# Performance work log

Hardware: AMD Instinct MI355X
Metric: run time of the kernel (lower is better)

Reference implementation:

```python
import jax, jax.numpy as jnp
import numpy as np

B, N, NC, T, C, H = 8, 16, 16, 64, 512, 8


def setup_inputs() -> dict:
    key = jax.random.key(0)
    ks = jax.random.split(key, 7)
    s = 1.0 / np.sqrt(C)  # ~kaiming-uniform scale for Linear weights
    x = jax.random.normal(ks[0], (B, N, T, C), dtype=jnp.float32)
    c = jax.random.normal(ks[1], (B, NC, T, C), dtype=jnp.float32)
    mask = jax.random.randint(ks[2], (B, N * T, (N + NC) * T), 0, 2).astype(bool)
    Wq = jax.random.normal(ks[3], (C, C), dtype=jnp.float32) * s  # [out, in], torch Linear layout
    Wk = jax.random.normal(ks[4], (C, C), dtype=jnp.float32) * s
    Wv = jax.random.normal(ks[5], (C, C), dtype=jnp.float32) * s
    Wp = jax.random.normal(ks[6], (C, C), dtype=jnp.float32) * s
    return {"x": x, "c": c, "mask": mask, "Wq": Wq, "Wk": Wk, "Wv": Wv, "Wp": Wp}


def reference(x, c, mask, Wq, Wk, Wv, Wp):
    Bx, Nx, Tx, Cx = x.shape
    Dh = Cx // H
    kv_in = jnp.concatenate([x, c], axis=1)           # hybrid: [B, N+NC, T, C]
    Nk = kv_in.shape[1]
    # torch Linear: y = x @ W.T  -> einsum '...c,dc->...d'
    q = jnp.einsum('bntc,dc->bntd', x, Wq).reshape(Bx, Nx * Tx, H, Dh).transpose(0, 2, 1, 3)
    k = jnp.einsum('bntc,dc->bntd', kv_in, Wk).reshape(Bx, Nk * Tx, H, Dh).transpose(0, 2, 1, 3)
    v = jnp.einsum('bntc,dc->bntd', kv_in, Wv).reshape(Bx, Nk * Tx, H, Dh).transpose(0, 2, 1, 3)
    att = jnp.einsum('bhqd,bhkd->bhqk', q, k) * (1.0 / np.sqrt(Dh))  # [B,H,NT,NkT]
    att = jnp.where(mask[:, None, :, :], -jnp.inf, att)
    att = jax.nn.softmax(att, axis=-1)
    y = jnp.einsum('bhqk,bhkd->bhqd', att, v)          # [B,H,NT,Dh]
    y = y.transpose(0, 2, 1, 3).reshape(Bx, Nx * Tx, Cx)
    y = jnp.einsum('btc,dc->btd', y, Wp)
    return y.reshape(Bx, Nx, Tx, Cx)
```

## Files before the change

### kernel.cpp

```cpp
#include <hip/hip_runtime.h>
#include <hip/hip_bf16.h>
#include <stdint.h>

typedef __bf16 v8bf __attribute__((ext_vector_type(8)));
typedef float f32x4 __attribute__((ext_vector_type(4)));

__device__ __forceinline__ void gload_lds16(const void* g, void* l) {
    __builtin_amdgcn_global_load_lds(
        (const __attribute__((address_space(1))) void*)g,
        (__attribute__((address_space(3))) void*)l, 16, 0, 0);
}

__device__ __forceinline__ unsigned short f2bf(float f) {
    __hip_bfloat16 h = __float2bfloat16(f);
    return __builtin_bit_cast(unsigned short, h);
}

__global__ __launch_bounds__(256) void cvt_xcw(const float* __restrict__ x,
                                               const float* __restrict__ c,
                                               const float* __restrict__ wq,
                                               const float* __restrict__ wk,
                                               const float* __restrict__ wv,
                                               const float* __restrict__ wp,
                                               __hip_bfloat16* __restrict__ xc,
                                               __hip_bfloat16* __restrict__ wout) {
    int bid = blockIdx.x;
    if (bid < 8192) {
        int i = bid * 256 + threadIdx.x;
        long e = (long)i * 4;
        int b = (int)(e >> 20);
        int rem = (int)(e & ((1 << 20) - 1));
        int r = rem >> 9;
        int col = rem & 511;
        const float* src = (r < 1024) ? (x + ((long)b << 19) + (long)r * 512 + col)
                                      : (c + ((long)b << 19) + (long)(r - 1024) * 512 + col);
        float4 v = *(const float4*)src;
        ushort4 o;
        o.x = f2bf(v.x); o.y = f2bf(v.y); o.z = f2bf(v.z); o.w = f2bf(v.w);
        ((ushort4*)xc)[i] = o;
    } else {
        int i = (bid - 8192) * 256 + threadIdx.x;
        int e = i * 4;
        int w = e >> 18;
        int off = e & ((1 << 18) - 1);
        const float* src = (w == 0 ? wq : w == 1 ? wk : w == 2 ? wv : wp) + off;
        float4 val = *(const float4*)src;
        ushort4 o;
        o.x = f2bf(val.x); o.y = f2bf(val.y); o.z = f2bf(val.z); o.w = f2bf(val.w);
        ((ushort4*)wout)[i] = o;
    }
}

__global__ __launch_bounds__(256) void cvt_mask(const int* __restrict__ mask,
                                                unsigned long long* __restrict__ mb) {
    int t = threadIdx.x;
    long base = (long)blockIdx.x * 1024;
#pragma unroll
    for (int j = 0; j < 4; j++) {
        long i = base + j * 256 + t;
        int v = mask[i] != 0;
        unsigned long long bits = __ballot(v);
        if ((t & 63) == 0) mb[i >> 6] = bits;
    }
}

__global__ __launch_bounds__(256) void gemm_qkv(const __hip_bfloat16* __restrict__ A,
                                                const __hip_bfloat16* __restrict__ Bw,
                                                __hip_bfloat16* __restrict__ Qw,
                                                __hip_bfloat16* __restrict__ Kw,
                                                __hip_bfloat16* __restrict__ Vtw) {
    __shared__ union {
        struct { __hip_bfloat16 As[128 * 32]; __hip_bfloat16 Bs[128 * 32]; } s;
        __hip_bfloat16 T[128 * 136];
    } u;
    const int tid = threadIdx.x;
    const int wave = tid >> 6, lane = tid & 63;
    const int m0 = blockIdx.x * 128, n0 = blockIdx.y * 128;

    const int la = lane >> 2;
    const int kc = (lane & 3) * 8;
    const long ga0 = (long)(m0 + wave * 16 + la) * 512 + kc;
    const long ga1 = (long)(m0 + (wave + 4) * 16 + la) * 512 + kc;
    const long gb0 = (long)(n0 + wave * 16 + la) * 512 + kc;
    const long gb1 = (long)(n0 + (wave + 4) * 16 + la) * 512 + kc;

    f32x4 acc[4][4] = {};
    const int mw = (wave & 1) * 64, nw = (wave >> 1) * 64;
    const int lrow = lane & 15, lk = (lane >> 4) * 8;

    for (int k0 = 0; k0 < 512; k0 += 32) {
        gload_lds16(A + ga0 + k0, &u.s.As[wave * 512]);
        gload_lds16(A + ga1 + k0, &u.s.As[(wave + 4) * 512]);
        gload_lds16(Bw + gb0 + k0, &u.s.Bs[wave * 512]);
        gload_lds16(Bw + gb1 + k0, &u.s.Bs[(wave + 4) * 512]);
        __syncthreads();
        v8bf a[4], b[4];
#pragma unroll
        for (int i = 0; i < 4; i++) {
            a[i] = *(const v8bf*)&u.s.As[(mw + i * 16 + lrow) * 32 + lk];
            b[i] = *(const v8bf*)&u.s.Bs[(nw + i * 16 + lrow) * 32 + lk];
        }
#pragma unroll
        for (int mi = 0; mi < 4; mi++)
#pragma unroll
            for (int ni = 0; ni < 4; ni++)
                acc[mi][ni] = __builtin_amdgcn_mfma_f32_16x16x32_bf16(a[mi], b[ni], acc[mi][ni], 0, 0, 0);
        __syncthreads();
    }

    const int lq = lane >> 4;
    if (blockIdx.y < 8) {
#pragma unroll
        for (int mi = 0; mi < 4; mi++)
#pragma unroll
            for (int ni = 0; ni < 4; ni++)
#pragma unroll
                for (int r = 0; r < 4; r++) {
                    int grow = m0 + mw + mi * 16 + lq * 4 + r;
                    int gcol = n0 + nw + ni * 16 + lrow;
                    int w = gcol >> 9, g9 = gcol & 511;
                    int h = g9 >> 6, dh = g9 & 63;
                    int b_ = grow >> 11, rr = grow & 2047;
                    __hip_bfloat16 bv = __float2bfloat16(acc[mi][ni][r]);
                    if (w == 0) {
                        if (rr < 1024)
                            Qw[((long)(b_ * 8 + h) * 1024 + rr) * 64 + dh] = bv;
                    } else {
                        Kw[((long)(b_ * 8 + h) * 2048 + rr) * 64 + dh] = bv;
                    }
                }
    } else {
#pragma unroll
        for (int mi = 0; mi < 4; mi++)
#pragma unroll
            for (int ni = 0; ni < 4; ni++) {
                int n_l = nw + ni * 16 + lrow;
                int m_l = mw + mi * 16 + lq * 4;
                ushort4 pk;
                pk.x = f2bf(acc[mi][ni][0]); pk.y = f2bf(acc[mi][ni][1]);
                pk.z = f2bf(acc[mi][ni][2]); pk.w = f2bf(acc[mi][ni][3]);
                *(ushort4*)&u.T[n_l * 136 + m_l] = pk;
            }
        __syncthreads();
        const int no = (blockIdx.y - 8) * 128;
        const int b_ = m0 >> 11, rrb = m0 & 2047;
#pragma unroll
        for (int i = 0; i < 8; i++) {
            int s = tid + i * 256;
            int n_l = s >> 4, ch = s & 15;
            int ng = no + n_l;
            int h = ng >> 6, dh = ng & 63;
            uint4 v = *(const uint4*)&u.T[n_l * 136 + ch * 8];
            *(uint4*)&Vtw[((long)(b_ * 8 + h) * 64 + dh) * 2048 + rrb + ch * 8] = v;
        }
    }
}

__global__ __launch_bounds__(256) void gemm_out(const __hip_bfloat16* __restrict__ A,
                                                const __hip_bfloat16* __restrict__ Bw,
                                                float* __restrict__ outp) {
    __shared__ __hip_bfloat16 As[128 * 32];
    __shared__ __hip_bfloat16 Bs[128 * 32];
    const int tid = threadIdx.x;
    const int wave = tid >> 6, lane = tid & 63;
    const int m0 = blockIdx.x * 128, n0 = blockIdx.y * 128;

    const int la = lane >> 2;
    const int kc = (lane & 3) * 8;
    const long ga0 = (long)(m0 + wave * 16 + la) * 512 + kc;
    const long ga1 = (long)(m0 + (wave + 4) * 16 + la) * 512 + kc;
    const long gb0 = (long)(n0 + wave * 16 + la) * 512 + kc;
    const long gb1 = (long)(n0 + (wave + 4) * 16 + la) * 512 + kc;

    f32x4 acc[4][4] = {};
    const int mw = (wave & 1) * 64, nw = (wave >> 1) * 64;
    const int lrow = lane & 15, lk = (lane >> 4) * 8;

    for (int k0 = 0; k0 < 512; k0 += 32) {
        gload_lds16(A + ga0 + k0, &As[wave * 512]);
        gload_lds16(A + ga1 + k0, &As[(wave + 4) * 512]);
        gload_lds16(Bw + gb0 + k0, &Bs[wave * 512]);
        gload_lds16(Bw + gb1 + k0, &Bs[(wave + 4) * 512]);
        __syncthreads();
        v8bf a[4], b[4];
#pragma unroll
        for (int i = 0; i < 4; i++) {
            a[i] = *(const v8bf*)&As[(mw + i * 16 + lrow) * 32 + lk];
            b[i] = *(const v8bf*)&Bs[(nw + i * 16 + lrow) * 32 + lk];
        }
#pragma unroll
        for (int mi = 0; mi < 4; mi++)
#pragma unroll
            for (int ni = 0; ni < 4; ni++)
                acc[mi][ni] = __builtin_amdgcn_mfma_f32_16x16x32_bf16(a[mi], b[ni], acc[mi][ni], 0, 0, 0);
        __syncthreads();
    }

    const int lq = lane >> 4;
#pragma unroll
    for (int mi = 0; mi < 4; mi++)
#pragma unroll
        for (int ni = 0; ni < 4; ni++)
#pragma unroll
            for (int r = 0; r < 4; r++) {
                int grow = m0 + mw + mi * 16 + lq * 4 + r;
                int gcol = n0 + nw + ni * 16 + lrow;
                outp[(long)grow * 512 + gcol] = acc[mi][ni][r];
            }
}

__global__ __launch_bounds__(256) void flash(const __hip_bfloat16* __restrict__ Q,
                                             const __hip_bfloat16* __restrict__ K,
                                             const __hip_bfloat16* __restrict__ Vt,
                                             const unsigned long long* __restrict__ Mb,
                                             __hip_bfloat16* __restrict__ Y) {
    __shared__ __hip_bfloat16 Ps[4][64 * 32];
    __shared__ float Ls[4][64];

    const int L = blockIdx.x;
    const int b = L & 7, h = L >> 7, qt = (L >> 3) & 15;
    const int bh = b * 8 + h;
    const int tid = threadIdx.x, w = tid >> 6, lane = tid & 63;
    const int lcol = lane & 15, lq = lane >> 4;

    const __hip_bfloat16* Qp = Q + ((long)bh * 1024 + qt * 64) * 64;
    const __hip_bfloat16* Kp = K + ((long)bh * 2048 + w * 16 + lcol) * 64;
    const __hip_bfloat16* Vp = Vt + (long)bh * 64 * 2048;
    const unsigned long long* Mp = Mb + ((long)b * 1024 + qt * 64) * 32;

    v8bf bq[4][2];
#pragma unroll
    for (int mi = 0; mi < 4; mi++)
#pragma unroll
        for (int ks = 0; ks < 2; ks++)
            bq[mi][ks] = *(const v8bf*)(Qp + (mi * 16 + lcol) * 64 + ks * 32 + lq * 8);

    f32x4 Oacc[4][4] = {};
    float lsum[4] = {0.f, 0.f, 0.f, 0.f};
    const int vkey = (lq >> 1) * 64 + w * 16 + (lq & 1) * 8;
    const int mshift = w * 16 + lq * 4;

    for (int kt = 0; kt < 16; kt++) {
        unsigned long long mb_[4][2];
#pragma unroll
        for (int mi = 0; mi < 4; mi++)
#pragma unroll
            for (int kt2 = 0; kt2 < 2; kt2++)
                mb_[mi][kt2] = Mp[(mi * 16 + lcol) * 32 + kt * 2 + kt2] >> mshift;

        v8bf ak[2][2];
#pragma unroll
        for (int kt2 = 0; kt2 < 2; kt2++)
#pragma unroll
            for (int ks = 0; ks < 2; ks++)
                ak[kt2][ks] = *(const v8bf*)(Kp + (long)(kt * 128 + kt2 * 64) * 64 + ks * 32 + lq * 8);

        v8bf bv[4];
#pragma unroll
        for (int nd = 0; nd < 4; nd++)
            bv[nd] = *(const v8bf*)(Vp + (long)(nd * 16 + lcol) * 2048 + kt * 128 + vkey);

#pragma unroll
        for (int kt2 = 0; kt2 < 2; kt2++)
#pragma unroll
            for (int mi = 0; mi < 4; mi++) {
                f32x4 st = {};
                st = __builtin_amdgcn_mfma_f32_16x16x32_bf16(ak[kt2][0], bq[mi][0], st, 0, 0, 0);
                st = __builtin_amdgcn_mfma_f32_16x16x32_bf16(ak[kt2][1], bq[mi][1], st, 0, 0, 0);
                ushort4 pk;
                float e;
#pragma unroll
                for (int r = 0; r < 4; r++) {
                    float s = fminf(st[r] * 0.125f, 40.f);
                    e = __expf(s);
                    e = ((mb_[mi][kt2] >> r) & 1ull) ? 0.f : e;
                    lsum[mi] += e;
                    ((unsigned short*)&pk)[r] = f2bf(e);
                }
                int row = mi * 16 + lcol;
                int ch = (kt2 * 2 + (lq >> 1)) ^ (row & 3);
                *(ushort4*)((char*)&Ps[w][0] + row * 64 + ch * 16 + (lq & 1) * 8) = pk;
            }

#pragma unroll
        for (int mi = 0; mi < 4; mi++) {
            int row = mi * 16 + lcol;
            v8bf ap = *(const v8bf*)((char*)&Ps[w][0] + row * 64 + ((lq ^ (row & 3)) * 16));
#pragma unroll
            for (int nd = 0; nd < 4; nd++)
                Oacc[mi][nd] = __builtin_amdgcn_mfma_f32_16x16x32_bf16(ap, bv[nd], Oacc[mi][nd], 0, 0, 0);
        }
    }

#pragma unroll
    for (int mi = 0; mi < 4; mi++) {
        float s = lsum[mi];
        s += __shfl_xor(s, 16);
        s += __shfl_xor(s, 32);
        lsum[mi] = s;
    }
    if (lq == 0) {
#pragma unroll
        for (int mi = 0; mi < 4; mi++) Ls[w][mi * 16 + lcol] = lsum[mi];
    }
    __syncthreads();

    float* Of = (float*)&Ps[0][0];
    if (w == 0) {
#pragma unroll
        for (int mi = 0; mi < 4; mi++)
#pragma unroll
            for (int nd = 0; nd < 4; nd++)
#pragma unroll
                for (int r = 0; r < 4; r++)
                    Of[(mi * 16 + lq * 4 + r) * 64 + nd * 16 + lcol] = Oacc[mi][nd][r];
    }
    __syncthreads();
    if (w == 1) {
#pragma unroll
        for (int mi = 0; mi < 4; mi++)
#pragma unroll
            for (int nd = 0; nd < 4; nd++)
#pragma unroll
                for (int r = 0; r < 4; r++) {
                    int idx = (mi * 16 + lq * 4 + r) * 64 + nd * 16 + lcol;
                    Of[idx] += Oacc[mi][nd][r];
                }
    }
    __syncthreads();
    if (w == 2) {
#pragma unroll
        for (int mi = 0; mi < 4; mi++)
#pragma unroll
            for (int nd = 0; nd < 4; nd++)
#pragma unroll
                for (int r = 0; r < 4; r++) {
                    int idx = (mi * 16 + lq * 4 + r) * 64 + nd * 16 + lcol;
                    Of[idx] += Oacc[mi][nd][r];
                }
    }
    __syncthreads();
    if (w == 3) {
#pragma unroll
        for (int mi = 0; mi < 4; mi++)
#pragma unroll
            for (int r = 0; r < 4; r++) {
                int q = mi * 16 + lq * 4 + r;
                float rs = Ls[0][q] + Ls[1][q] + Ls[2][q] + Ls[3][q];
                float inv = 1.f / rs;
                long row = (long)b * 1024 + qt * 64 + q;
#pragma unroll
                for (int nd = 0; nd < 4; nd++) {
                    int idx = q * 64 + nd * 16 + lcol;
                    float val = (Oacc[mi][nd][r] + Of[idx]) * inv;
                    Y[row * 512 + h * 64 + nd * 16 + lcol] = __float2bfloat16(val);
                }
            }
    }
}

extern "C" void kernel_launch(void* const* d_in, const int* in_sizes, int n_in,
                              void* d_out, int out_size, void* d_ws, size_t ws_size,
                              hipStream_t stream) {
    const float* x = (const float*)d_in[0];
    const float* c = (const float*)d_in[1];
    const int* mask = (const int*)d_in[2];
    const float* Wq = (const float*)d_in[3];
    const float* Wk = (const float*)d_in[4];
    const float* Wv = (const float*)d_in[5];
    const float* Wp = (const float*)d_in[6];

    char* ws = (char*)d_ws;
    __hip_bfloat16* xc  = (__hip_bfloat16*)(ws);
    __hip_bfloat16* Wbf = (__hip_bfloat16*)(ws + 16777216);
    __hip_bfloat16* Qw  = (__hip_bfloat16*)(ws + 18874368);
    __hip_bfloat16* Kw  = (__hip_bfloat16*)(ws + 27262976);
    __hip_bfloat16* Vtw = (__hip_bfloat16*)(ws + 44040192);
    __hip_bfloat16* Yb  = (__hip_bfloat16*)(ws + 60817408);
    unsigned long long* Mbp = (unsigned long long*)(ws);

    cvt_xcw<<<9216, 256, 0, stream>>>(x, c, Wq, Wk, Wv, Wp, xc, Wbf);
    gemm_qkv<<<dim3(128, 12), 256, 0, stream>>>(xc, Wbf, Qw, Kw, Vtw);
    cvt_mask<<<16384, 256, 0, stream>>>(mask, Mbp);
    flash<<<1024, 256, 0, stream>>>(Qw, Kw, Vtw, Mbp, Yb);
    gemm_out<<<dim3(64, 4), 256, 0, stream>>>(Yb, Wbf + 3 * 262144, (float*)d_out);
}
```

Measured before the change: 297.2 us.

## Share P tile across warps, split PV by head-dim, fold scale into Q

The flash kernel now writes every warp's exp-score slice into one shared 64x128 P tile, and each warp computes output for its own 16 head-dim columns across all keys. This replaces the per-warp key split that needed a serialized four-stage LDS reduction of O partials. It removes that reduction and three quarters of the O accumulator registers, but adds two block-wide barriers per key tile. The 1/sqrt(Dh) scale is also folded into Q at projection time, which drops a multiply per score element.

```diff
diff --git a/kernel.cpp b/kernel.cpp
--- a/kernel.cpp
+++ b/kernel.cpp
@@ -121,12 +121,13 @@
                     int w = gcol >> 9, g9 = gcol & 511;
                     int h = g9 >> 6, dh = g9 & 63;
                     int b_ = grow >> 11, rr = grow & 2047;
-                    __hip_bfloat16 bv = __float2bfloat16(acc[mi][ni][r]);
+                    float val = acc[mi][ni][r];
                     if (w == 0) {
                         if (rr < 1024)
-                            Qw[((long)(b_ * 8 + h) * 1024 + rr) * 64 + dh] = bv;
+                            Qw[((long)(b_ * 8 + h) * 1024 + rr) * 64 + dh] =
+                                __float2bfloat16(val * 0.125f);
                     } else {
-                        Kw[((long)(b_ * 8 + h) * 2048 + rr) * 64 + dh] = bv;
+                        Kw[((long)(b_ * 8 + h) * 2048 + rr) * 64 + dh] = __float2bfloat16(val);
                     }
                 }
     } else {
@@ -214,7 +215,7 @@
                                              const __hip_bfloat16* __restrict__ Vt,
                                              const unsigned long long* __restrict__ Mb,
                                              __hip_bfloat16* __restrict__ Y) {
-    __shared__ __hip_bfloat16 Ps[4][64 * 32];
+    __shared__ __hip_bfloat16 Ps[64 * 128];
     __shared__ float Ls[4][64];
 
     const int L = blockIdx.x;
@@ -225,7 +226,7 @@
 
     const __hip_bfloat16* Qp = Q + ((long)bh * 1024 + qt * 64) * 64;
     const __hip_bfloat16* Kp = K + ((long)bh * 2048 + w * 16 + lcol) * 64;
-    const __hip_bfloat16* Vp = Vt + (long)bh * 64 * 2048;
+    const __hip_bfloat16* Vp = Vt + ((long)bh * 64 + w * 16 + lcol) * 2048;
     const unsigned long long* Mp = Mb + ((long)b * 1024 + qt * 64) * 32;
 
     v8bf bq[4][2];
@@ -235,9 +236,8 @@
         for (int ks = 0; ks < 2; ks++)
             bq[mi][ks] = *(const v8bf*)(Qp + (mi * 16 + lcol) * 64 + ks * 32 + lq * 8);
 
-    f32x4 Oacc[4][4] = {};
+    f32x4 Oacc[4] = {};
     float lsum[4] = {0.f, 0.f, 0.f, 0.f};
-    const int vkey = (lq >> 1) * 64 + w * 16 + (lq & 1) * 8;
     const int mshift = w * 16 + lq * 4;
 
     for (int kt = 0; kt < 16; kt++) {
@@ -254,11 +254,6 @@
 #pragma unroll
             for (int ks = 0; ks < 2; ks++)
                 ak[kt2][ks] = *(const v8bf*)(Kp + (long)(kt * 128 + kt2 * 64) * 64 + ks * 32 + lq * 8);
-
-        v8bf bv[4];
-#pragma unroll
-        for (int nd = 0; nd < 4; nd++)
-            bv[nd] = *(const v8bf*)(Vp + (long)(nd * 16 + lcol) * 2048 + kt * 128 + vkey);
 
 #pragma unroll
         for (int kt2 = 0; kt2 < 2; kt2++)
@@ -268,28 +263,36 @@
                 st = __builtin_amdgcn_mfma_f32_16x16x32_bf16(ak[kt2][0], bq[mi][0], st, 0, 0, 0);
                 st = __builtin_amdgcn_mfma_f32_16x16x32_bf16(ak[kt2][1], bq[mi][1], st, 0, 0, 0);
                 ushort4 pk;
-                float e;
 #pragma unroll
                 for (int r = 0; r < 4; r++) {
-                    float s = fminf(st[r] * 0.125f, 40.f);
-                    e = __expf(s);
+                    float s = fminf(st[r], 40.f);
+                    float e = __expf(s);
                     e = ((mb_[mi][kt2] >> r) & 1ull) ? 0.f : e;
                     lsum[mi] += e;
                     ((unsigned short*)&pk)[r] = f2bf(e);
                 }
-                int row = mi * 16 + lcol;
-                int ch = (kt2 * 2 + (lq >> 1)) ^ (row & 3);
-                *(ushort4*)((char*)&Ps[w][0] + row * 64 + ch * 16 + (lq & 1) * 8) = pk;
+                int q = mi * 16 + lcol;
+                int ch = (kt2 * 8 + w * 2 + (lq >> 1)) ^ (q & 7);
+                *(ushort4*)((char*)Ps + q * 256 + ch * 16 + (lq & 1) * 8) = pk;
             }
 
+        v8bf bv[4];
+#pragma unroll
+        for (int kc = 0; kc < 4; kc++)
+            bv[kc] = *(const v8bf*)(Vp + kt * 128 + kc * 32 + lq * 8);
+
+        __syncthreads();
+
 #pragma unroll
         for (int mi = 0; mi < 4; mi++) {
-            int row = mi * 16 + lcol;
-            v8bf ap = *(const v8bf*)((char*)&Ps[w][0] + row * 64 + ((lq ^ (row & 3)) * 16));
-#pragma unroll
-            for (int nd = 0; nd < 4; nd++)
-                Oacc[mi][nd] = __builtin_amdgcn_mfma_f32_16x16x32_bf16(ap, bv[nd], Oacc[mi][nd], 0, 0, 0);
-        }
+            int q = mi * 16 + lcol;
+#pragma unroll
+            for (int kc = 0; kc < 4; kc++) {
+                v8bf ap = *(const v8bf*)((char*)Ps + q * 256 + (((kc * 4 + lq) ^ (q & 7)) * 16));
+                Oacc[mi] = __builtin_amdgcn_mfma_f32_16x16x32_bf16(ap, bv[kc], Oacc[mi], 0, 0, 0);
+            }
+        }
+        __syncthreads();
     }
 
 #pragma unroll
@@ -305,57 +308,16 @@
     }
     __syncthreads();
 
-    float* Of = (float*)&Ps[0][0];
-    if (w == 0) {
-#pragma unroll
-        for (int mi = 0; mi < 4; mi++)
-#pragma unroll
-            for (int nd = 0; nd < 4; nd++)
-#pragma unroll
-                for (int r = 0; r < 4; r++)
-                    Of[(mi * 16 + lq * 4 + r) * 64 + nd * 16 + lcol] = Oacc[mi][nd][r];
-    }
-    __syncthreads();
-    if (w == 1) {
-#pragma unroll
-        for (int mi = 0; mi < 4; mi++)
-#pragma unroll
-            for (int nd = 0; nd < 4; nd++)
-#pragma unroll
-                for (int r = 0; r < 4; r++) {
-                    int idx = (mi * 16 + lq * 4 + r) * 64 + nd * 16 + lcol;
-                    Of[idx] += Oacc[mi][nd][r];
-                }
-    }
-    __syncthreads();
-    if (w == 2) {
-#pragma unroll
-        for (int mi = 0; mi < 4; mi++)
-#pragma unroll
-            for (int nd = 0; nd < 4; nd++)
-#pragma unroll
-                for (int r = 0; r < 4; r++) {
-                    int idx = (mi * 16 + lq * 4 + r) * 64 + nd * 16 + lcol;
-                    Of[idx] += Oacc[mi][nd][r];
-                }
-    }
-    __syncthreads();
-    if (w == 3) {
-#pragma unroll
-        for (int mi = 0; mi < 4; mi++)
-#pragma unroll
-            for (int r = 0; r < 4; r++) {
-                int q = mi * 16 + lq * 4 + r;
-                float rs = Ls[0][q] + Ls[1][q] + Ls[2][q] + Ls[3][q];
-                float inv = 1.f / rs;
-                long row = (long)b * 1024 + qt * 64 + q;
-#pragma unroll
-                for (int nd = 0; nd < 4; nd++) {
-                    int idx = q * 64 + nd * 16 + lcol;
-                    float val = (Oacc[mi][nd][r] + Of[idx]) * inv;
-                    Y[row * 512 + h * 64 + nd * 16 + lcol] = __float2bfloat16(val);
-                }
-            }
+#pragma unroll
+    for (int mi = 0; mi < 4; mi++) {
+#pragma unroll
+        for (int r = 0; r < 4; r++) {
+            int q = mi * 16 + lq * 4 + r;
+            float rs = Ls[0][q] + Ls[1][q] + Ls[2][q] + Ls[3][q];
+            float inv = 1.f / rs;
+            long row = (long)b * 1024 + qt * 64 + q;
+            Y[row * 512 + h * 64 + w * 16 + lcol] = __float2bfloat16(Oacc[mi][r] * inv);
+        }
     }
 }
 
```

Measured after the change: 317.0 us. 6.7% more time.
